# Kernel tuning notes

Measured on AMD Instinct MI355X. Metric: run time of the kernel, lower is better.

The kernel has to match this reference:

```python
import jax, jax.numpy as jnp
import numpy as np

N_EMBD = 2048
N_Q = 32
N_KV = 8
GROUP = N_Q // N_KV   # 4
HD = N_EMBD // N_Q    # 64
BASE = 10000.0
NEG_INF = -1e30


def _rope(x):
    """Rotate-half RoPE on last dim; positions 1..t along dim -2 (as in the
    original _build_cache which uses arange(1, seq_len+1))."""
    t, d = x.shape[-2], x.shape[-1]
    d2 = d // 2
    theta = 1.0 / (BASE ** (jnp.arange(0, d, 2, dtype=jnp.float32) / d))  # (d/2,)
    pos = jnp.arange(1, t + 1, dtype=jnp.float32)                          # (t,)
    ang = pos[:, None] * theta[None, :]                                    # (t, d/2)
    ang = jnp.concatenate([ang, ang], axis=-1)                             # (t, d)
    sin, cos = jnp.sin(ang), jnp.cos(ang)
    rot = jnp.concatenate([-x[..., d2:], x[..., :d2]], axis=-1)
    return x * cos + rot * sin


def setup_inputs() -> dict:
    key = jax.random.key(0)
    ks = jax.random.split(key, 5)
    b, t = 2, 1024
    s = 1.0 / np.sqrt(N_EMBD)
    return {
        "x": jax.random.normal(ks[0], (b, t, N_EMBD), dtype=jnp.float32),
        "wq": jax.random.normal(ks[1], (N_EMBD, N_EMBD), dtype=jnp.float32) * s,
        "bq": jnp.zeros((N_EMBD,), dtype=jnp.float32),
        "wk": jax.random.normal(ks[2], (N_EMBD, N_KV * HD), dtype=jnp.float32) * s,
        "bk": jnp.zeros((N_KV * HD,), dtype=jnp.float32),
        "wv": jax.random.normal(ks[3], (N_EMBD, N_KV * HD), dtype=jnp.float32) * s,
        "bv": jnp.zeros((N_KV * HD,), dtype=jnp.float32),
        "wo": jax.random.normal(ks[4], (N_EMBD, N_EMBD), dtype=jnp.float32) * s,
        "bo": jnp.zeros((N_EMBD,), dtype=jnp.float32),
    }


def reference(x, wq, bq, wk, bk, wv, bv, wo, bo):
    b, t, _ = x.shape
    q = x @ wq + bq                                   # (b, t, E)
    k = x @ wk + bk                                   # (b, t, NKV*HD)
    v = x @ wv + bv
    q = q.reshape(b, t, N_Q, HD).transpose(0, 2, 1, 3)        # (b, nq, t, d)
    q = q.reshape(b, N_KV, GROUP, t, HD)                      # (b, hkv, g, t, d)
    k = k.reshape(b, t, N_KV, HD).transpose(0, 2, 1, 3)       # (b, hkv, t, d)
    v = v.reshape(b, t, N_KV, HD).transpose(0, 2, 1, 3)
    q = _rope(q)
    k = _rope(k)
    scale = jnp.sqrt(jnp.float32(HD))
    att = jnp.einsum("bhgqd,bhkd->bhgqk", q, k) / scale       # (b, hkv, g, t, t)
    causal = jnp.tril(jnp.ones((t, t), dtype=bool))
    att = jnp.where(causal, att, NEG_INF)
    att = jax.nn.softmax(att, axis=-1)
    out = jnp.einsum("bhgqk,bhkd->bhgqd", att, v)             # (b, hkv, g, t, d)
    out = out.transpose(0, 3, 1, 2, 4).reshape(b, t, N_EMBD)  # (b, t, E)
    return out @ wo + bo
```

## Files before the change

### kernel.cpp

```cpp
#include <hip/hip_runtime.h>
#include <hip/hip_bf16.h>
#include <cstdint>


typedef __attribute__((ext_vector_type(8))) short short8;
typedef __attribute__((ext_vector_type(4))) short short4v;
typedef __attribute__((ext_vector_type(4))) float f32x4;

__device__ inline short f2b(float f) {
  union { float f; unsigned u; } v; v.f = f;
  unsigned r = v.u + 0x7fffu + ((v.u >> 16) & 1u);
  return (short)(r >> 16);
}

__device__ inline float exp2_fast(float x) {
  float r;
  asm("v_exp_f32 %0, %1" : "=v"(r) : "v"(x));
  return r;
}

__device__ inline void gl_lds16(const void* g, void* l) {
  __builtin_amdgcn_global_load_lds((const __attribute__((address_space(1))) void*)g,
                                   (__attribute__((address_space(3))) void*)l,
                                   16, 0, 0);
}

__global__ void prep_kernel(const float* __restrict__ x,
                            const float* __restrict__ wq, const float* __restrict__ wk,
                            const float* __restrict__ wv, const float* __restrict__ wo,
                            short* __restrict__ xb, short* __restrict__ WqkvT,
                            short* __restrict__ woT, int nCast) {
  const int bx = blockIdx.x;
  const int tid = threadIdx.x;
  if (bx < nCast) {
    int i = bx * 256 + tid;
    float4 v = ((const float4*)x)[i];
    short4v o; o.x = f2b(v.x); o.y = f2b(v.y); o.z = f2b(v.z); o.w = f2b(v.w);
    ((short4v*)xb)[i] = o;
    return;
  }
  __shared__ float tile[64][65];
  const int id = bx - nCast;
  const int wx = id % 80, ky = id / 80;
  const float* W; short* WT; int N, off, nb;
  if (wx < 32)      { W = wq; WT = WqkvT; N = 2048; off = 0;    nb = wx * 64; }
  else if (wx < 40) { W = wk; WT = WqkvT; N = 512;  off = 2048; nb = (wx - 32) * 64; }
  else if (wx < 48) { W = wv; WT = WqkvT; N = 512;  off = 2560; nb = (wx - 40) * 64; }
  else              { W = wo; WT = woT;   N = 2048; off = 0;    nb = (wx - 48) * 64; }
  const int kb = ky * 64;
  const int c = tid & 63, r0 = tid >> 6;
#pragma unroll
  for (int s = 0; s < 16; ++s) {
    int k = r0 + s * 4;
    tile[c][k] = W[(size_t)(kb + k) * N + nb + c];
  }
  __syncthreads();
#pragma unroll
  for (int s = 0; s < 16; ++s) {
    int n = r0 + s * 4;
    WT[(size_t)(off + nb + n) * 2048 + kb + c] = f2b(tile[n][c]);
  }
}

__device__ __forceinline__ void gemm_loop_bk64(const short* __restrict__ Ag,
                                               const short* __restrict__ Bg,
                                               short* lA, short* lB,
                                               int w, int l15, int q4,
                                               f32x4 acc[2][4]) {
  const int K = 2048, NS = 32;
  auto stage = [&](int s, int d) {
    const short* As = Ag + s * 64;
    const short* Bs = Bg + s * 64;
    short* a = lA + d * 8192 + w * 512;
    gl_lds16(As, a);
    gl_lds16(As + 64 * K, a + 2048);
    gl_lds16(As + 32, a + 4096);
    gl_lds16(As + 64 * K + 32, a + 6144);
    short* bp = lB + d * 4096 + w * 512;
    gl_lds16(Bs, bp);
    gl_lds16(Bs + 32, bp + 2048);
  };
  stage(0, 0);
  for (int s = 0; s < NS; ++s) {
    const int d = s & 1;
    __syncthreads();
    if (s + 1 < NS) stage(s + 1, d ^ 1);
#pragma unroll
    for (int ks = 0; ks < 2; ++ks) {
      const short* ap = lA + d * 8192 + ks * 4096;
      const short* bp = lB + d * 4096 + ks * 2048;
      short8 af[2], bf[4];
#pragma unroll
      for (int mf = 0; mf < 2; ++mf) af[mf] = *(const short8*)(ap + (w * 32 + mf * 16 + l15) * 32 + q4 * 8);
#pragma unroll
      for (int nf = 0; nf < 4; ++nf) bf[nf] = *(const short8*)(bp + (nf * 16 + l15) * 32 + q4 * 8);
#pragma unroll
      for (int mf = 0; mf < 2; ++mf)
#pragma unroll
        for (int nf = 0; nf < 4; ++nf)
          acc[mf][nf] = __builtin_amdgcn_mfma_f32_16x16x32_bf16(af[mf], bf[nf], acc[mf][nf], 0, 0, 0);
    }
  }
}

__launch_bounds__(256, 3)
__global__ void gemm_qkv(const short* __restrict__ A, const short* __restrict__ BT,
                         const float* __restrict__ bq, const float* __restrict__ bk,
                         const float* __restrict__ bv,
                         short* __restrict__ Qb, short* __restrict__ Kb,
                         short* __restrict__ VTb) {
  __shared__ __align__(16) short lA[16384];
  __shared__ __align__(16) short lB[8192];
  const int K = 2048;
  const int tid = threadIdx.x, lane = tid & 63, w = tid >> 6;
  const int q4 = lane >> 4, l15 = lane & 15;
  const int bn = blockIdx.x * 64, bm = blockIdx.y * 128;

  const short* Ag = A + (size_t)(bm + (tid >> 2)) * K + ((tid & 3) << 3);
  const short* Bg = BT + (size_t)(bn + (tid >> 2)) * K + ((tid & 3) << 3);

  f32x4 acc[2][4];
  const f32x4 fz = {0.f, 0.f, 0.f, 0.f};
#pragma unroll
  for (int i = 0; i < 2; ++i)
#pragma unroll
    for (int j = 0; j < 4; ++j) acc[i][j] = fz;

  gemm_loop_bk64(Ag, Bg, lA, lB, w, l15, q4, acc);

  const float L2T = 0.4152410118609203f;
  const float theta_a = exp2_fast(-(float)l15 * L2T);
  const float theta_b = exp2_fast(-(float)(l15 + 16) * L2T);
  const float s2 = 0.18033688011112042f;

  if (bn < 2048) {
    const int h = bn >> 6;
    float bb0 = bq[bn + l15], bb1 = bq[bn + 16 + l15], bb2 = bq[bn + 32 + l15], bb3 = bq[bn + 48 + l15];
#pragma unroll
    for (int mf = 0; mf < 2; ++mf)
#pragma unroll
      for (int r = 0; r < 4; ++r) {
        int row = bm + w * 32 + mf * 16 + q4 * 4 + r;
        int batch = row >> 10, t = row & 1023;
        float pos = (float)(t + 1);
        float sa, ca, sb, cb;
        __sincosf(pos * theta_a, &sa, &ca);
        __sincosf(pos * theta_b, &sb, &cb);
        float x0 = acc[mf][0][r] + bb0, x2 = acc[mf][2][r] + bb2;
        float x1 = acc[mf][1][r] + bb1, x3 = acc[mf][3][r] + bb3;
        size_t base = ((size_t)(batch * 32 + h) * 1024 + t) * 64;
        Qb[base + l15]      = f2b((x0 * ca - x2 * sa) * s2);
        Qb[base + l15 + 32] = f2b((x2 * ca + x0 * sa) * s2);
        Qb[base + l15 + 16] = f2b((x1 * cb - x3 * sb) * s2);
        Qb[base + l15 + 48] = f2b((x3 * cb + x1 * sb) * s2);
      }
  } else if (bn < 2560) {
    const int co = bn - 2048;
    const int hkv = co >> 6;
    float bb0 = bk[co + l15], bb1 = bk[co + 16 + l15], bb2 = bk[co + 32 + l15], bb3 = bk[co + 48 + l15];
#pragma unroll
    for (int mf = 0; mf < 2; ++mf)
#pragma unroll
      for (int r = 0; r < 4; ++r) {
        int row = bm + w * 32 + mf * 16 + q4 * 4 + r;
        int batch = row >> 10, t = row & 1023;
        float pos = (float)(t + 1);
        float sa, ca, sb, cb;
        __sincosf(pos * theta_a, &sa, &ca);
        __sincosf(pos * theta_b, &sb, &cb);
        float x0 = acc[mf][0][r] + bb0, x2 = acc[mf][2][r] + bb2;
        float x1 = acc[mf][1][r] + bb1, x3 = acc[mf][3][r] + bb3;
        size_t base = (size_t)(batch * 8 + hkv) * 65536 + t * 32;
        Kb[base + l15]              = f2b(x0 * ca - x2 * sa);
        Kb[base + l15 + 16]         = f2b(x1 * cb - x3 * sb);
        Kb[base + 32768 + l15]      = f2b(x2 * ca + x0 * sa);
        Kb[base + 32768 + l15 + 16] = f2b(x3 * cb + x1 * sb);
      }
  } else {
    const int co = bn - 2560;
    const int hkv = co >> 6;
    float bb[4];
#pragma unroll
    for (int nf = 0; nf < 4; ++nf) bb[nf] = bv[co + nf * 16 + l15];
#pragma unroll
    for (int mf = 0; mf < 2; ++mf) {
      int row0 = bm + w * 32 + mf * 16 + q4 * 4;
      int batch = row0 >> 10, t0 = row0 & 1023;
      size_t base = (size_t)(batch * 8 + hkv) * 65536 + (size_t)(t0 >> 5) * 2048 + (t0 & 31);
#pragma unroll
      for (int nf = 0; nf < 4; ++nf) {
        short4v pk;
#pragma unroll
        for (int r = 0; r < 4; ++r) pk[r] = f2b(acc[mf][nf][r] + bb[nf]);
        *(short4v*)(VTb + base + (nf * 16 + l15) * 32) = pk;
      }
    }
  }
}

#define PROW 72
__launch_bounds__(256, 3)
__global__ void attn6_kernel(const short* __restrict__ Qb, const short* __restrict__ Kb,
                             const short* __restrict__ VTb, short* __restrict__ AO) {
  __shared__ __align__(16) short lK[2][4096];
  __shared__ __align__(16) short lV[2][4096];
  __shared__ __align__(16) short lP[4][16 * PROW];
  const int tid = threadIdx.x, lane = tid & 63, w = tid >> 6;
  const int q4 = lane >> 4, l15 = lane & 15;
  const int qt = (int)gridDim.x - 1 - (int)blockIdx.x;
  const int h = blockIdx.y, b = blockIdx.z;
  const int hkv = h >> 2;
  const int qb = qt * 128 + w * 32;
  const int kdiag = qb >> 6;
  const int ns = qt * 2 + 2;

  const short* Qg = Qb + (size_t)(b * 32 + h) * 65536;
  const short* Kg = Kb + (size_t)(b * 8 + hkv) * 65536;
  const short* Vg = VTb + (size_t)(b * 8 + hkv) * 65536;
  short* lPw = lP[w];

  short8 qf[2][2];
#pragma unroll
  for (int mf = 0; mf < 2; ++mf) {
    const short* qr = Qg + (size_t)(qb + mf * 16 + l15) * 64 + q4 * 8;
    qf[mf][0] = *(const short8*)(qr);
    qf[mf][1] = *(const short8*)(qr + 32);
  }

  const f32x4 fz = {0.f, 0.f, 0.f, 0.f};
  f32x4 o[2][4], ol[2];
#pragma unroll
  for (int mf = 0; mf < 2; ++mf) {
    ol[mf] = fz;
#pragma unroll
    for (int i = 0; i < 4; ++i) o[mf][i] = fz;
  }
  short8 ones;
#pragma unroll
  for (int i = 0; i < 8; ++i) ones[i] = (short)0x3F80;

  auto stage = [&](int s, int d) {
#pragma unroll
    for (int c = 0; c < 4; ++c) {
      int j = w * 4 + c;
      if (j < 8) {
        const short* src = Kg + (size_t)(j >> 2) * 32768 + s * 2048 + (j & 3) * 512 + lane * 8;
        gl_lds16(src, &lK[d][j * 512]);
      } else {
        int jj = j - 8;
        const short* src = Vg + (size_t)(s * 2 + (jj >> 2)) * 2048 + (jj & 3) * 512 + lane * 8;
        gl_lds16(src, &lV[d][jj * 512]);
      }
    }
  };

  stage(0, 0);
  for (int s = 0; s < ns; ++s) {
    const int d = s & 1;
    __syncthreads();
    if (s + 1 < ns) stage(s + 1, d ^ 1);
    if (s <= kdiag) {
      short8 kf0[4], kf1[4], vf0[4], vf1[4];
#pragma unroll
      for (int nt = 0; nt < 4; ++nt) {
        kf0[nt] = *(const short8*)(&lK[d][(nt * 16 + l15) * 32 + q4 * 8]);
        kf1[nt] = *(const short8*)(&lK[d][2048 + (nt * 16 + l15) * 32 + q4 * 8]);
        vf0[nt] = *(const short8*)(&lV[d][(nt * 16 + l15) * 32 + q4 * 8]);
        vf1[nt] = *(const short8*)(&lV[d][2048 + (nt * 16 + l15) * 32 + q4 * 8]);
      }
      const bool diag = (s == kdiag);
#pragma unroll
      for (int mf = 0; mf < 2; ++mf) {
        f32x4 sv[4];
#pragma unroll
        for (int nt = 0; nt < 4; ++nt) {
          f32x4 z = __builtin_amdgcn_mfma_f32_16x16x32_bf16(qf[mf][0], kf0[nt], fz, 0, 0, 0);
          sv[nt] = __builtin_amdgcn_mfma_f32_16x16x32_bf16(qf[mf][1], kf1[nt], z, 0, 0, 0);
        }
        if (diag) {
#pragma unroll
          for (int r = 0; r < 4; ++r) {
            const int qrow = qb + mf * 16 + q4 * 4 + r;
            const int col = s * 64 + l15;
#pragma unroll
            for (int nt = 0; nt < 4; ++nt)
              if (col + nt * 16 > qrow) sv[nt][r] = -1e30f;
          }
        }
#pragma unroll
        for (int r = 0; r < 4; ++r)
#pragma unroll
          for (int nt = 0; nt < 4; ++nt)
            lPw[(q4 * 4 + r) * PROW + nt * 16 + l15] = f2b(exp2_fast(sv[nt][r] - 16.f));

        short8 pf0 = *(const short8*)(lPw + l15 * PROW + q4 * 8);
        short8 pf1 = *(const short8*)(lPw + l15 * PROW + 32 + q4 * 8);
        ol[mf] = __builtin_amdgcn_mfma_f32_16x16x32_bf16(pf0, ones, ol[mf], 0, 0, 0);
        ol[mf] = __builtin_amdgcn_mfma_f32_16x16x32_bf16(pf1, ones, ol[mf], 0, 0, 0);
#pragma unroll
        for (int dt = 0; dt < 4; ++dt) {
          o[mf][dt] = __builtin_amdgcn_mfma_f32_16x16x32_bf16(pf0, vf0[dt], o[mf][dt], 0, 0, 0);
          o[mf][dt] = __builtin_amdgcn_mfma_f32_16x16x32_bf16(pf1, vf1[dt], o[mf][dt], 0, 0, 0);
        }
      }
    }
  }

#pragma unroll
  for (int mf = 0; mf < 2; ++mf)
#pragma unroll
    for (int r = 0; r < 4; ++r) {
      float inv = __builtin_amdgcn_rcpf(ol[mf][r]);
      int row = qb + mf * 16 + q4 * 4 + r;
#pragma unroll
      for (int dt = 0; dt < 4; ++dt)
        AO[(size_t)(b * 1024 + row) * 2048 + h * 64 + dt * 16 + l15] = f2b(o[mf][dt][r] * inv);
    }
}

__launch_bounds__(256, 3)
__global__ void gemm_out(const short* __restrict__ A, const short* __restrict__ BT,
                         float* __restrict__ C, const float* __restrict__ bias,
                         int N, int K) {
  __shared__ __align__(16) short lA[16384];
  __shared__ __align__(16) short lB[8192];
  const int tid = threadIdx.x, lane = tid & 63, w = tid >> 6;
  const int q4 = lane >> 4, l15 = lane & 15;
  const int bn = blockIdx.x * 64, bm = blockIdx.y * 128;

  const short* Ag = A + (size_t)(bm + (tid >> 2)) * K + ((tid & 3) << 3);
  const short* Bg = BT + (size_t)(bn + (tid >> 2)) * K + ((tid & 3) << 3);

  f32x4 acc[2][4];
  const f32x4 fz = {0.f, 0.f, 0.f, 0.f};
#pragma unroll
  for (int i = 0; i < 2; ++i)
#pragma unroll
    for (int j = 0; j < 4; ++j) acc[i][j] = fz;

  gemm_loop_bk64(Ag, Bg, lA, lB, w, l15, q4, acc);

#pragma unroll
  for (int mf = 0; mf < 2; ++mf)
#pragma unroll
    for (int nf = 0; nf < 4; ++nf) {
      int col = bn + nf * 16 + l15;
      float bb = bias[col];
#pragma unroll
      for (int r = 0; r < 4; ++r) {
        int row = bm + w * 32 + mf * 16 + q4 * 4 + r;
        C[(size_t)row * N + col] = acc[mf][nf][r] + bb;
      }
    }
}

extern "C" void kernel_launch(void* const* d_in, const int* in_sizes, int n_in,
                              void* d_out, int out_size, void* d_ws, size_t ws_size,
                              hipStream_t stream) {
  const float* x  = (const float*)d_in[0];
  const float* wq = (const float*)d_in[1];
  const float* bq = (const float*)d_in[2];
  const float* wk = (const float*)d_in[3];
  const float* bk = (const float*)d_in[4];
  const float* wv = (const float*)d_in[5];
  const float* bv = (const float*)d_in[6];
  const float* wo = (const float*)d_in[7];
  const float* bo = (const float*)d_in[8];
  float* out = (float*)d_out;
  const int B = in_sizes[0] / (1024 * 2048);
  const int M = B * 1024;

  char* ws = (char*)d_ws;
  size_t off = 0;
  auto alloc = [&](size_t bytes) -> char* {
    char* p = ws + off;
    off += (bytes + 255) & ~(size_t)255;
    return p;
  };
  short* xb    = (short*)alloc((size_t)M * 2048 * 2);
  short* WqkvT = (short*)alloc((size_t)3072 * 2048 * 2);
  short* woT   = (short*)alloc((size_t)2048 * 2048 * 2);
  short* Qb    = (short*)alloc((size_t)B * 32 * 1024 * 64 * 2);
  short* Kb    = (short*)alloc((size_t)B * 8 * 2 * 1024 * 32 * 2);
  short* VTb   = (short*)alloc((size_t)B * 8 * 32 * 64 * 32 * 2);
  short* AO    = (short*)alloc((size_t)M * 2048 * 2);

  const int nCast = M * 2048 / 1024;
  prep_kernel<<<nCast + 80 * 32, 256, 0, stream>>>(x, wq, wk, wv, wo, xb, WqkvT, woT, nCast);
  gemm_qkv<<<dim3(48, M / 128), 256, 0, stream>>>(xb, WqkvT, bq, bk, bv, Qb, Kb, VTb);
  attn6_kernel<<<dim3(8, 32, B), 256, 0, stream>>>(Qb, Kb, VTb, AO);
  gemm_out<<<dim3(32, M / 128), 256, 0, stream>>>(AO, woT, out, bo, 2048, 2048);
}
```

Baseline: 210.5 us.

## Store GEMM operands, K and V in 8-element-chunked tiled layouts for conflict-free LDS

The producers (cast, weight transpose, QKV epilogue, attention output) now write bf16 data in a blocked layout of 64 rows by 8 k-elements per 1 KiB chunk. Each global_load_lds then copies a contiguous chunk, and the MFMA fragment reads from LDS become 16-byte accesses at a stride of 8 shorts instead of 32. The goal is to remove LDS bank conflicts in the GEMM and attention inner loops and make the global loads fully contiguous. In exchange, the scattered stores in the producers and epilogues become less coalesced (for example, the 2-byte K and AO writes).

```diff
diff --git a/kernel.cpp b/kernel.cpp
--- a/kernel.cpp
+++ b/kernel.cpp
@@ -35,8 +35,11 @@
   if (bx < nCast) {
     int i = bx * 256 + tid;
     float4 v = ((const float4*)x)[i];
+    int f0 = i * 4;
+    int row = f0 >> 11, k = f0 & 2047;
     short4v o; o.x = f2b(v.x); o.y = f2b(v.y); o.z = f2b(v.z); o.w = f2b(v.w);
-    ((short4v*)xb)[i] = o;
+    size_t addr = ((size_t)(row >> 6) * 256 + (k >> 3)) * 512 + (row & 63) * 8 + (k & 7);
+    *(short4v*)(xb + addr) = o;
     return;
   }
   __shared__ float tile[64][65];
@@ -57,43 +60,49 @@
   __syncthreads();
 #pragma unroll
   for (int s = 0; s < 16; ++s) {
-    int n = r0 + s * 4;
-    WT[(size_t)(off + nb + n) * 2048 + kb + c] = f2b(tile[n][c]);
-  }
-}
-
-__device__ __forceinline__ void gemm_loop_bk64(const short* __restrict__ Ag,
-                                               const short* __restrict__ Bg,
+    int n_abs = off + nb + r0 + s * 4;
+    int k = kb + c;
+    WT[((size_t)(n_abs >> 6) * 256 + (k >> 3)) * 512 + (n_abs & 63) * 8 + (k & 7)] =
+        f2b(tile[r0 + s * 4][c]);
+  }
+}
+
+__device__ __forceinline__ void gemm_loop_bk64(const short* __restrict__ Ag0,
+                                               const short* __restrict__ Bg0,
                                                short* lA, short* lB,
-                                               int w, int l15, int q4,
+                                               int w, int lane, int l15, int q4,
                                                f32x4 acc[2][4]) {
-  const int K = 2048, NS = 32;
+  const int NS = 32;
   auto stage = [&](int s, int d) {
-    const short* As = Ag + s * 64;
-    const short* Bs = Bg + s * 64;
-    short* a = lA + d * 8192 + w * 512;
-    gl_lds16(As, a);
-    gl_lds16(As + 64 * K, a + 2048);
-    gl_lds16(As + 32, a + 4096);
-    gl_lds16(As + 64 * K + 32, a + 6144);
-    short* bp = lB + d * 4096 + w * 512;
-    gl_lds16(Bs, bp);
-    gl_lds16(Bs + 32, bp + 2048);
+#pragma unroll
+    for (int c = 0; c < 4; ++c) {
+      int p = w * 4 + c;
+      const short* src = Ag0 + ((size_t)(p >> 3) * 256 + s * 8 + (p & 7)) * 512 + lane * 8;
+      gl_lds16(src, lA + d * 8192 + p * 512);
+    }
+#pragma unroll
+    for (int c = 0; c < 2; ++c) {
+      int q = w * 2 + c;
+      const short* src = Bg0 + (size_t)(s * 8 + q) * 512 + lane * 8;
+      gl_lds16(src, lB + d * 4096 + q * 512);
+    }
   };
   stage(0, 0);
+  const int rb = w >> 1;
+  const int r64 = (w & 1) * 32;
   for (int s = 0; s < NS; ++s) {
     const int d = s & 1;
     __syncthreads();
     if (s + 1 < NS) stage(s + 1, d ^ 1);
 #pragma unroll
     for (int ks = 0; ks < 2; ++ks) {
-      const short* ap = lA + d * 8192 + ks * 4096;
-      const short* bp = lB + d * 4096 + ks * 2048;
+      const short* ap = lA + d * 8192 + (rb * 8 + ks * 4 + q4) * 512 + (r64 + l15) * 8;
+      const short* bp = lB + d * 4096 + (ks * 4 + q4) * 512 + l15 * 8;
       short8 af[2], bf[4];
 #pragma unroll
-      for (int mf = 0; mf < 2; ++mf) af[mf] = *(const short8*)(ap + (w * 32 + mf * 16 + l15) * 32 + q4 * 8);
-#pragma unroll
-      for (int nf = 0; nf < 4; ++nf) bf[nf] = *(const short8*)(bp + (nf * 16 + l15) * 32 + q4 * 8);
+      for (int mf = 0; mf < 2; ++mf) af[mf] = *(const short8*)(ap + mf * 128);
+#pragma unroll
+      for (int nf = 0; nf < 4; ++nf) bf[nf] = *(const short8*)(bp + nf * 128);
 #pragma unroll
       for (int mf = 0; mf < 2; ++mf)
 #pragma unroll
@@ -111,13 +120,12 @@
                          short* __restrict__ VTb) {
   __shared__ __align__(16) short lA[16384];
   __shared__ __align__(16) short lB[8192];
-  const int K = 2048;
   const int tid = threadIdx.x, lane = tid & 63, w = tid >> 6;
   const int q4 = lane >> 4, l15 = lane & 15;
   const int bn = blockIdx.x * 64, bm = blockIdx.y * 128;
 
-  const short* Ag = A + (size_t)(bm + (tid >> 2)) * K + ((tid & 3) << 3);
-  const short* Bg = BT + (size_t)(bn + (tid >> 2)) * K + ((tid & 3) << 3);
+  const short* Ag0 = A + (size_t)(bm >> 6) * 131072;
+  const short* Bg0 = BT + (size_t)(bn >> 6) * 131072;
 
   f32x4 acc[2][4];
   const f32x4 fz = {0.f, 0.f, 0.f, 0.f};
@@ -126,7 +134,7 @@
 #pragma unroll
     for (int j = 0; j < 4; ++j) acc[i][j] = fz;
 
-  gemm_loop_bk64(Ag, Bg, lA, lB, w, l15, q4, acc);
+  gemm_loop_bk64(Ag0, Bg0, lA, lB, w, lane, l15, q4, acc);
 
   const float L2T = 0.4152410118609203f;
   const float theta_a = exp2_fast(-(float)l15 * L2T);
@@ -158,6 +166,7 @@
     const int co = bn - 2048;
     const int hkv = co >> 6;
     float bb0 = bk[co + l15], bb1 = bk[co + 16 + l15], bb2 = bk[co + 32 + l15], bb3 = bk[co + 48 + l15];
+    const int dq0 = l15 >> 3, j = l15 & 7;
 #pragma unroll
     for (int mf = 0; mf < 2; ++mf)
 #pragma unroll
@@ -170,11 +179,11 @@
         __sincosf(pos * theta_b, &sb, &cb);
         float x0 = acc[mf][0][r] + bb0, x2 = acc[mf][2][r] + bb2;
         float x1 = acc[mf][1][r] + bb1, x3 = acc[mf][3][r] + bb3;
-        size_t base = (size_t)(batch * 8 + hkv) * 65536 + t * 32;
-        Kb[base + l15]              = f2b(x0 * ca - x2 * sa);
-        Kb[base + l15 + 16]         = f2b(x1 * cb - x3 * sb);
-        Kb[base + 32768 + l15]      = f2b(x2 * ca + x0 * sa);
-        Kb[base + 32768 + l15 + 16] = f2b(x3 * cb + x1 * sb);
+        size_t base = (size_t)(batch * 8 + hkv) * 65536 + (size_t)t * 8 + j;
+        Kb[base + (size_t)(dq0)     * 8192] = f2b(x0 * ca - x2 * sa);
+        Kb[base + (size_t)(dq0 + 2) * 8192] = f2b(x1 * cb - x3 * sb);
+        Kb[base + (size_t)(dq0 + 4) * 8192] = f2b(x2 * ca + x0 * sa);
+        Kb[base + (size_t)(dq0 + 6) * 8192] = f2b(x3 * cb + x1 * sb);
       }
   } else {
     const int co = bn - 2560;
@@ -186,13 +195,14 @@
     for (int mf = 0; mf < 2; ++mf) {
       int row0 = bm + w * 32 + mf * 16 + q4 * 4;
       int batch = row0 >> 10, t0 = row0 & 1023;
-      size_t base = (size_t)(batch * 8 + hkv) * 65536 + (size_t)(t0 >> 5) * 2048 + (t0 & 31);
+      size_t base = (size_t)(batch * 8 + hkv) * 65536 + ((size_t)(t0 >> 3) * 64) * 8 + (t0 & 7);
 #pragma unroll
       for (int nf = 0; nf < 4; ++nf) {
+        int d = nf * 16 + l15;
         short4v pk;
 #pragma unroll
         for (int r = 0; r < 4; ++r) pk[r] = f2b(acc[mf][nf][r] + bb[nf]);
-        *(short4v*)(VTb + base + (nf * 16 + l15) * 32) = pk;
+        *(short4v*)(VTb + base + d * 8) = pk;
       }
     }
   }
@@ -244,12 +254,12 @@
     for (int c = 0; c < 4; ++c) {
       int j = w * 4 + c;
       if (j < 8) {
-        const short* src = Kg + (size_t)(j >> 2) * 32768 + s * 2048 + (j & 3) * 512 + lane * 8;
+        const short* src = Kg + ((size_t)j * 1024 + s * 64 + lane) * 8;
         gl_lds16(src, &lK[d][j * 512]);
       } else {
-        int jj = j - 8;
-        const short* src = Vg + (size_t)(s * 2 + (jj >> 2)) * 2048 + (jj & 3) * 512 + lane * 8;
-        gl_lds16(src, &lV[d][jj * 512]);
+        int tq = j - 8;
+        const short* src = Vg + ((size_t)(s * 8 + tq) * 64 + lane) * 8;
+        gl_lds16(src, &lV[d][tq * 512]);
       }
     }
   };
@@ -263,10 +273,10 @@
       short8 kf0[4], kf1[4], vf0[4], vf1[4];
 #pragma unroll
       for (int nt = 0; nt < 4; ++nt) {
-        kf0[nt] = *(const short8*)(&lK[d][(nt * 16 + l15) * 32 + q4 * 8]);
-        kf1[nt] = *(const short8*)(&lK[d][2048 + (nt * 16 + l15) * 32 + q4 * 8]);
-        vf0[nt] = *(const short8*)(&lV[d][(nt * 16 + l15) * 32 + q4 * 8]);
-        vf1[nt] = *(const short8*)(&lV[d][2048 + (nt * 16 + l15) * 32 + q4 * 8]);
+        kf0[nt] = *(const short8*)(&lK[d][q4 * 512 + (nt * 16 + l15) * 8]);
+        kf1[nt] = *(const short8*)(&lK[d][(4 + q4) * 512 + (nt * 16 + l15) * 8]);
+        vf0[nt] = *(const short8*)(&lV[d][q4 * 512 + (nt * 16 + l15) * 8]);
+        vf1[nt] = *(const short8*)(&lV[d][(4 + q4) * 512 + (nt * 16 + l15) * 8]);
       }
       const bool diag = (s == kdiag);
 #pragma unroll
@@ -311,10 +321,13 @@
 #pragma unroll
     for (int r = 0; r < 4; ++r) {
       float inv = __builtin_amdgcn_rcpf(ol[mf][r]);
-      int row = qb + mf * 16 + q4 * 4 + r;
-#pragma unroll
-      for (int dt = 0; dt < 4; ++dt)
-        AO[(size_t)(b * 1024 + row) * 2048 + h * 64 + dt * 16 + l15] = f2b(o[mf][dt][r] * inv);
+      int row = b * 1024 + qb + mf * 16 + q4 * 4 + r;
+#pragma unroll
+      for (int dt = 0; dt < 4; ++dt) {
+        int col = h * 64 + dt * 16 + l15;
+        AO[((size_t)(row >> 6) * 256 + (col >> 3)) * 512 + (row & 63) * 8 + (col & 7)] =
+            f2b(o[mf][dt][r] * inv);
+      }
     }
 }
 
@@ -328,8 +341,8 @@
   const int q4 = lane >> 4, l15 = lane & 15;
   const int bn = blockIdx.x * 64, bm = blockIdx.y * 128;
 
-  const short* Ag = A + (size_t)(bm + (tid >> 2)) * K + ((tid & 3) << 3);
-  const short* Bg = BT + (size_t)(bn + (tid >> 2)) * K + ((tid & 3) << 3);
+  const short* Ag0 = A + (size_t)(bm >> 6) * 131072;
+  const short* Bg0 = BT + (size_t)(bn >> 6) * 131072;
 
   f32x4 acc[2][4];
   const f32x4 fz = {0.f, 0.f, 0.f, 0.f};
@@ -338,7 +351,7 @@
 #pragma unroll
     for (int j = 0; j < 4; ++j) acc[i][j] = fz;
 
-  gemm_loop_bk64(Ag, Bg, lA, lB, w, l15, q4, acc);
+  gemm_loop_bk64(Ag0, Bg0, lA, lB, w, lane, l15, q4, acc);
 
 #pragma unroll
   for (int mf = 0; mf < 2; ++mf)
@@ -381,10 +394,9 @@
   short* WqkvT = (short*)alloc((size_t)3072 * 2048 * 2);
   short* woT   = (short*)alloc((size_t)2048 * 2048 * 2);
   short* Qb    = (short*)alloc((size_t)B * 32 * 1024 * 64 * 2);
-  short* Kb    = (short*)alloc((size_t)B * 8 * 2 * 1024 * 32 * 2);
-  short* VTb   = (short*)alloc((size_t)B * 8 * 32 * 64 * 32 * 2);
+  short* Kb    = (short*)alloc((size_t)B * 8 * 8 * 1024 * 8 * 2);
+  short* VTb   = (short*)alloc((size_t)B * 8 * 128 * 64 * 8 * 2);
   short* AO    = (short*)alloc((size_t)M * 2048 * 2);
-
   const int nCast = M * 2048 / 1024;
   prep_kernel<<<nCast + 80 * 32, 256, 0, stream>>>(x, wq, wk, wv, wo, xb, WqkvT, woT, nCast);
   gemm_qkv<<<dim3(48, M / 128), 256, 0, stream>>>(xb, WqkvT, bq, bk, bv, Qb, Kb, VTb);
```

New measurement: 217.7 us. 3.4% more time.
